# Optimization experiments

Measured on AMD Instinct MI355X. Metric: run time of the kernel, lower is better.

Reference implementation:

```python
import jax, jax.numpy as jnp
import numpy as np

GC_ALPHA = 3.0  # saturation factor in MTGNN-style graph constructor
TOP_K = 5       # ctor arg: GraphConstructor(n_classes, 5, dim)
EPS_NORM = 1e-12


def setup_inputs() -> dict:
    key = jax.random.key(0)
    k1, k2, k3, k4, k5 = jax.random.split(key, 5)
    B, C, H, W = 32, 384, 80, 80
    N = 27
    return {
        "x": jax.random.normal(k1, (B, C, H, W), dtype=jnp.float32),
        "alpha": jnp.ones((), dtype=jnp.float32),
        "clusters": jax.random.normal(k2, (N, C), dtype=jnp.float32),
        "gc_w1": jax.random.normal(k3, (C, C), dtype=jnp.float32) / np.sqrt(C),
        "gc_w2": jax.random.normal(k4, (C, C), dtype=jnp.float32) / np.sqrt(C),
        "gcn_w": jax.random.normal(k5, (C, C), dtype=jnp.float32) / np.sqrt(C),
    }


def _refine_clusters(clusters, gc_w1, gc_w2, gcn_w):
    # GraphConstructor: learned asymmetric adjacency over n_classes nodes, top-k sparsified
    n = clusters.shape[0]
    a = jnp.tanh(GC_ALPHA * (clusters @ gc_w1))          # [n, d]
    b = jnp.tanh(GC_ALPHA * (clusters @ gc_w2))          # [n, d]
    adj = jax.nn.relu(jnp.tanh(GC_ALPHA * (a @ b.T - b @ a.T)))  # [n, n]
    topv, _ = jax.lax.top_k(adj, TOP_K)
    A = jnp.where(adj >= topv[:, -1:], adj, 0.0)         # keep top-k per row
    # GCNConv (no bias): add self-loops, symmetric normalization
    A_hat = A + jnp.eye(n, dtype=A.dtype)
    dinv = 1.0 / jnp.sqrt(A_hat.sum(axis=1))
    A_norm = dinv[:, None] * A_hat * dinv[None, :]
    return A_norm @ (clusters @ gcn_w)                   # [n, d]


def reference(x, alpha, clusters, gc_w1, gc_w2, gcn_w):
    # mp=True path: refine codebook with tiny GCN over learned graph
    cl = _refine_clusters(clusters, gc_w1, gc_w2, gcn_w)
    # cosine similarity of per-pixel features against codebook
    nc = cl / jnp.maximum(jnp.linalg.norm(cl, axis=1, keepdims=True), EPS_NORM)
    nf = x / jnp.maximum(jnp.linalg.norm(x, axis=1, keepdims=True), EPS_NORM)
    inner_products = jnp.einsum('bchw,nc->bnhw', nf, nc)          # [B, n, H, W]
    cluster_probs = jax.nn.softmax(inner_products * alpha, axis=1)
    cluster_loss = -(cluster_probs * inner_products).sum(axis=1).mean()
    # entropy over unnormalized similarities (computed in original forward)
    p = jax.nn.softmax(jnp.einsum('bchw,nc->bnhw', x, clusters), axis=1)
    entropy = (-(p * jnp.log(p + 1e-10)).sum(axis=1)).mean()
    return cluster_loss, inner_products, cl, entropy
```

## Files before the change

kernel.cpp:

```cpp
#include <hip/hip_runtime.h>
#include <math.h>

#define N_CL   27
#define C_DIM  384
#define HW_SZ  6400
#define B_SZ   32
#define NPIX   (B_SZ*HW_SZ)
#define NTILE  3200
#define NCHUNK 12
#define WSF_PARTS 24576
#define WSF_ADJ   40000
#define ENT_OFF (1 + (size_t)NPIX*N_CL + (size_t)N_CL*C_DIM)

typedef unsigned short ushort_t;
using bf16x8 = __attribute__((ext_vector_type(8))) short;
using f32x4  = __attribute__((ext_vector_type(4))) float;

__device__ __forceinline__ float xla_tanh_f32(float x) {
    const float c = 7.99881172180175781f;
    if (fabsf(x) < 0.0004f) return x;
    const float xc = fminf(fmaxf(x, -c), c);
    const float x2 = xc*xc;
    float p = fmaf(x2, -2.76076847742355e-16f, 2.00018790482477e-13f);
    p = fmaf(x2, p, -8.60467152213735e-11f);
    p = fmaf(x2, p,  5.12229709037114e-08f);
    p = fmaf(x2, p,  1.48572235717979e-05f);
    p = fmaf(x2, p,  6.37261928875436e-04f);
    p = fmaf(x2, p,  4.89352455891786e-03f);
    p = xc*p;
    float q = fmaf(x2, 1.19825839466702e-06f, 1.18534705686654e-04f);
    q = fmaf(x2, q, 2.26843463243900e-03f);
    q = fmaf(x2, q, 4.89352518554385e-03f);
    return p/q;
}

__global__ __launch_bounds__(384) void cl_refine_mm(const float* __restrict__ clusters,
                                                    const float* __restrict__ w1,
                                                    const float* __restrict__ w2,
                                                    const float* __restrict__ w3,
                                                    float* __restrict__ ws) {
    const int i = blockIdx.x;
    const int m = blockIdx.y;
    const int j = threadIdx.x;
    __shared__ float crow[C_DIM];
    crow[j] = clusters[i*C_DIM + j];
    __syncthreads();
    const float* __restrict__ W = (m==0) ? w1 : (m==1) ? w2 : w3;
    float s0=0.f,s1=0.f,s2=0.f,s3=0.f;
    #pragma unroll 4
    for (int k=0;k<C_DIM;k+=4){
        s0 = fmaf(crow[k+0], W[(size_t)(k+0)*C_DIM + j], s0);
        s1 = fmaf(crow[k+1], W[(size_t)(k+1)*C_DIM + j], s1);
        s2 = fmaf(crow[k+2], W[(size_t)(k+2)*C_DIM + j], s2);
        s3 = fmaf(crow[k+3], W[(size_t)(k+3)*C_DIM + j], s3);
    }
    const float acc = (s0+s1)+(s2+s3);
    ws[(size_t)m*N_CL*C_DIM + i*C_DIM + j] = (m<2) ? xla_tanh_f32(3.0f*acc) : acc;
}

__global__ __launch_bounds__(64) void cl_adj(const float* __restrict__ ws,
                                             float* __restrict__ adj_out) {
    const float* __restrict__ Am = ws;
    const float* __restrict__ Bm = ws + N_CL*C_DIM;
    const int i = blockIdx.x / N_CL, j = blockIdx.x - (blockIdx.x / N_CL)*N_CL;
    const int lane = threadIdx.x;
    float p=0.f, q=0.f;
    #pragma unroll
    for (int e=0;e<6;e++){
        const int k = e*64 + lane;
        p = fmaf(Am[i*C_DIM+k], Bm[j*C_DIM+k], p);
        q = fmaf(Bm[i*C_DIM+k], Am[j*C_DIM+k], q);
    }
    float d = p - q;
    #pragma unroll
    for (int m=1;m<64;m<<=1) d += __shfl_xor(d, m);
    if (lane==0) adj_out[blockIdx.x] = fmaxf(xla_tanh_f32(3.0f*d), 0.f);
}

__global__ __launch_bounds__(1024) void cl_graph2(float* ws,
                                                  const float* __restrict__ clusters_g,
                                                  float* __restrict__ out) {
    const float* cg = ws + 2*N_CL*C_DIM;
    float* cl_out = out + 1 + (size_t)NPIX*N_CL;
    const int t = threadIdx.x;

    __shared__ float anorm[N_CL][N_CL+1];
    __shared__ float dinv[N_CL];
    __shared__ float rinv[N_CL];
    __shared__ float cls[N_CL][C_DIM];

    if (t < N_CL*N_CL) {
        const int i = t / N_CL, j = t - (t / N_CL)*N_CL;
        anorm[i][j] = ws[WSF_ADJ + t];
    }
    __syncthreads();
    if (t < N_CL) {
        unsigned mask=0; float thr=0.f;
        for (int s=0;s<5;s++){
            float bv=-1.f; int bi2=0;
            for (int j=0;j<N_CL;j++){
                if (mask & (1u<<j)) continue;
                const float v = anorm[t][j];
                if (v > bv){ bv=v; bi2=j; }
            }
            mask |= 1u<<bi2; thr = bv;
        }
        float rs=0.f;
        for (int j=0;j<N_CL;j++){
            float v = anorm[t][j];
            v = (v >= thr) ? v : 0.f;
            if (j==t) v += 1.f;
            anorm[t][j] = v;
            rs += v;
        }
        dinv[t] = 1.0f / sqrtf(rs);
    }
    __syncthreads();
    if (t < N_CL*N_CL) {
        const int i = t / N_CL, j = t - (t / N_CL)*N_CL;
        anorm[i][j] = dinv[i]*anorm[i][j]*dinv[j];
    }
    __syncthreads();
    for (int idx=t; idx<N_CL*C_DIM; idx+=1024){
        const int i = idx / C_DIM, d = idx - i*C_DIM;
        float s=0.f;
        #pragma unroll
        for (int j=0;j<N_CL;j++) s = fmaf(anorm[i][j], cg[(size_t)j*C_DIM + d], s);
        cls[i][d] = s;
        cl_out[idx] = s;
    }
    __syncthreads();
    if (t < N_CL) {
        float ssq=0.f;
        for (int d=0; d<C_DIM; d++){ const float v=cls[t][d]; ssq=fmaf(v,v,ssq); }
        rinv[t] = 1.0f / fmaxf(sqrtf(ssq), 1e-12f);
    }
    __syncthreads();
    ushort_t* wpk = (ushort_t*)ws;
    for (int idx=t; idx<64*C_DIM; idx+=1024){
        const int n = idx / C_DIM, k = idx - n*C_DIM;
        float v = 0.f;
        if (n < N_CL) v = cls[n][k] * rinv[n];
        else if (n >= 32 && n < 32+N_CL) v = clusters_g[(size_t)(n-32)*C_DIM + k];
        const unsigned bits = __float_as_uint(v);
        const ushort_t hi = (ushort_t)(bits >> 16);
        const float lof = v - __uint_as_float(bits & 0xFFFF0000u);
        const ushort_t lo = (ushort_t)(__float_as_uint(lof) >> 16);
        wpk[idx] = hi;
        wpk[64*C_DIM + idx] = lo;
    }
}

__global__ __launch_bounds__(256, 4) void cl_mfma(const float* __restrict__ x,
                                                  const float* __restrict__ alpha_p,
                                                  const ushort_t* __restrict__ wpk,
                                                  float* __restrict__ ws,
                                                  float* __restrict__ out) {
    __shared__ float    lA[2][64][33];
    __shared__ __align__(16) ushort_t lB[2][2][64][40];
    __shared__ float redL[4], redE[4];

    const int tid = threadIdx.x;
    const int blk = blockIdx.x;
    const int b   = blk / 100;
    const int hw0 = (blk - b*100) * 64;
    const float* __restrict__ xb = x + (size_t)b*C_DIM*HW_SZ + hw0;

    const int lane = tid & 63;
    const int w    = tid >> 6;
    const int l15  = lane & 15;
    const int g    = lane >> 4;
    const int k0   = g*8;
    const int apx  = w*16 + l15;

    const int a_kk = tid >> 4;
    const int a_px = (tid & 15) * 4;
    const int b_n  = tid >> 2;
    const int b_kb = (tid & 3) * 8;

    float4 ra0, ra1; uint4 rb0, rb1;
    #define LOADR(c) {                                                            \
        const int ch = (c)*32;                                                    \
        ra0 = *(const float4*)(xb + (size_t)(ch      + a_kk)*HW_SZ + a_px);       \
        ra1 = *(const float4*)(xb + (size_t)(ch + 16 + a_kk)*HW_SZ + a_px);       \
        rb0 = *(const uint4*)(wpk + (size_t)(     b_n)*C_DIM + ch + b_kb);        \
        rb1 = *(const uint4*)(wpk + (size_t)(64 + b_n)*C_DIM + ch + b_kb); }
    #define WRITE(bf) {                                                           \
        lA[bf][a_px+0][a_kk]    = ra0.x; lA[bf][a_px+1][a_kk]    = ra0.y;         \
        lA[bf][a_px+2][a_kk]    = ra0.z; lA[bf][a_px+3][a_kk]    = ra0.w;         \
        lA[bf][a_px+0][a_kk+16] = ra1.x; lA[bf][a_px+1][a_kk+16] = ra1.y;         \
        lA[bf][a_px+2][a_kk+16] = ra1.z; lA[bf][a_px+3][a_kk+16] = ra1.w;         \
        *(uint4*)(&lB[bf][0][b_n][b_kb]) = rb0;                                   \
        *(uint4*)(&lB[bf][1][b_n][b_kb]) = rb1; }

    f32x4 acc0={0,0,0,0}, acc1={0,0,0,0}, acc2={0,0,0,0}, acc3={0,0,0,0};
    float ss = 0.f;

    LOADR(0);
    WRITE(0);
    LOADR(1);
    __syncthreads();

    for (int c = 0; c < NCHUNK; c++) {
        const int cur = c & 1;
        union { ushort_t u[8]; bf16x8 v; } Ah, Al;
        #pragma unroll
        for (int e = 0; e < 8; e++) {
            const float xv = lA[cur][apx][k0 + e];
            const unsigned bits = __float_as_uint(xv);
            Ah.u[e] = (ushort_t)(bits >> 16);
            const float lof = xv - __uint_as_float(bits & 0xFFFF0000u);
            Al.u[e] = (ushort_t)(__float_as_uint(lof) >> 16);
            ss = fmaf(xv, xv, ss);
        }
        #pragma unroll
        for (int t = 0; t < 4; t++) {
            union { uint4 q; bf16x8 v; } Bh, Bl;
            Bh.q = *(const uint4*)(&lB[cur][0][t*16 + l15][k0]);
            Bl.q = *(const uint4*)(&lB[cur][1][t*16 + l15][k0]);
            f32x4 a;
            a = (t==0)?acc0:(t==1)?acc1:(t==2)?acc2:acc3;
            a = __builtin_amdgcn_mfma_f32_16x16x32_bf16(Ah.v, Bh.v, a, 0,0,0);
            a = __builtin_amdgcn_mfma_f32_16x16x32_bf16(Ah.v, Bl.v, a, 0,0,0);
            a = __builtin_amdgcn_mfma_f32_16x16x32_bf16(Al.v, Bh.v, a, 0,0,0);
            if (t==0) acc0=a; else if (t==1) acc1=a; else if (t==2) acc2=a; else acc3=a;
        }
        __syncthreads();
        if (c + 1 < NCHUNK) {
            WRITE(cur ^ 1);
            if (c + 2 < NCHUNK) LOADR(c+2);
            __syncthreads();
        }
    }

    ss += __shfl_xor(ss, 16);
    ss += __shfl_xor(ss, 32);
    f32x4 invv;
    #pragma unroll
    for (int r = 0; r < 4; r++) {
        const float s2 = __shfl(ss, g*4 + r);
        invv[r] = 1.0f / fmaxf(sqrtf(s2), 1e-12f);
    }

    const float alpha = alpha_p[0];
    float* __restrict__ out1 = out + 1;
    const int pxb = hw0 + w*16 + g*4;

    f32x4 st0, st1;
    #pragma unroll
    for (int r=0;r<4;r++){ st0[r] = acc0[r]*invv[r]; st1[r] = acc1[r]*invv[r]; }
    *(f32x4*)(out1 + (size_t)b*N_CL*HW_SZ + (size_t)l15*HW_SZ + pxb) = st0;
    if (l15 <= 10)
        *(f32x4*)(out1 + (size_t)b*N_CL*HW_SZ + (size_t)(16+l15)*HW_SZ + pxb) = st1;

    float wloss = 0.f, went = 0.f;
    #pragma unroll
    for (int r=0;r<4;r++){
        const float ip0 = st0[r], ip1 = st1[r];
        const float v0 = alpha*ip0;
        const float v1 = (l15<=10) ? alpha*ip1 : -INFINITY;
        float mx = fmaxf(v0, v1);
        #pragma unroll
        for (int m=1;m<16;m<<=1) mx = fmaxf(mx, __shfl_xor(mx, m));
        const float e0 = expf(v0 - mx);
        const float e1 = (l15<=10) ? expf(v1 - mx) : 0.f;
        float z = e0 + e1;
        float tt = fmaf(e0, ip0, (l15<=10) ? e1*ip1 : 0.f);
        #pragma unroll
        for (int m=1;m<16;m<<=1){ z += __shfl_xor(z,m); tt += __shfl_xor(tt,m); }
        wloss += tt/z;
        const float c0 = acc2[r];
        const float c1 = (l15<=10) ? acc3[r] : -INFINITY;
        float emx = fmaxf(c0, c1);
        #pragma unroll
        for (int m=1;m<16;m<<=1) emx = fmaxf(emx, __shfl_xor(emx, m));
        const float f0 = expf(c0 - emx);
        const float f1 = (l15<=10) ? expf(c1 - emx) : 0.f;
        float ez = f0 + f1;
        #pragma unroll
        for (int m=1;m<16;m<<=1) ez += __shfl_xor(ez,m);
        const float iz = 1.0f/ez;
        const float p0 = f0*iz, p1 = f1*iz;
        float te = -p0*logf(p0+1e-10f) - p1*logf(p1+1e-10f);
        #pragma unroll
        for (int m=1;m<16;m<<=1) te += __shfl_xor(te,m);
        went += te;
    }
    wloss += __shfl_xor(wloss,16); wloss += __shfl_xor(wloss,32);
    went  += __shfl_xor(went ,16); went  += __shfl_xor(went ,32);
    if (lane == 0) { redL[w] = wloss; redE[w] = went; }
    __syncthreads();
    if (tid == 0) {
        float* parts = ws + WSF_PARTS;
        parts[blk]         = redL[0]+redL[1]+redL[2]+redL[3];
        parts[NTILE + blk] = redE[0]+redE[1]+redE[2]+redE[3];
    }
}

__global__ __launch_bounds__(1024) void cl_final_reduce(const float* __restrict__ ws,
                                                        float* __restrict__ out) {
    __shared__ float r[1024];
    const int t = threadIdx.x;
    const float* parts = ws + WSF_PARTS;
    float s = 0.f;
    for (int j=t; j<NTILE; j+=1024) s += parts[j];
    r[t] = s; __syncthreads();
    for (int sft=512;sft>0;sft>>=1){ if (t<sft) r[t]+=r[t+sft]; __syncthreads(); }
    if (t==0) out[0] = -r[0]*(1.0f/NPIX);
    __syncthreads();
    s = 0.f;
    for (int j=t; j<NTILE; j+=1024) s += parts[NTILE + j];
    r[t] = s; __syncthreads();
    for (int sft=512;sft>0;sft>>=1){ if (t<sft) r[t]+=r[t+sft]; __syncthreads(); }
    if (t==0) out[ENT_OFF] = r[0]*(1.0f/NPIX);
}

extern "C" void kernel_launch(void* const* d_in, const int* in_sizes, int n_in,
                              void* d_out, int out_size, void* d_ws, size_t ws_size,
                              hipStream_t stream) {
    const float* x        = (const float*)d_in[0];
    const float* alpha    = (const float*)d_in[1];
    const float* clusters = (const float*)d_in[2];
    const float* w1       = (const float*)d_in[3];
    const float* w2       = (const float*)d_in[4];
    const float* w3       = (const float*)d_in[5];
    float* out = (float*)d_out;
    float* ws  = (float*)d_ws;

    cl_refine_mm<<<dim3(27,3), dim3(384), 0, stream>>>(clusters, w1, w2, w3, ws);
    cl_adj<<<dim3(N_CL*N_CL), dim3(64), 0, stream>>>(ws, ws + WSF_ADJ);
    cl_graph2<<<dim3(1), dim3(1024), 0, stream>>>(ws, clusters, out);
    cl_mfma<<<dim3(NTILE), dim3(256), 0, stream>>>(x, alpha, (const ushort_t*)ws, ws, out);
    cl_final_reduce<<<dim3(1), dim3(1024), 0, stream>>>(ws, out);
}
```

Before: 136.9 us.

## Load x activations directly into registers, bypassing LDS transpose staging

The x tile is no longer staged through a shared-memory transpose buffer. Each lane now loads its own 8 channel values per chunk straight from global memory into registers, using scalar strided loads that are coalesced across pixels. Only the weight tile is still staged in LDS, and the loop is unrolled by two with ping-pong register sets. This removes the LDS writes and reads for A and some bank conflicts, at the cost of more global load instructions (scalar instead of float4) and higher register pressure.

```diff
diff --git a/kernel.cpp b/kernel.cpp
--- a/kernel.cpp
+++ b/kernel.cpp
@@ -156,7 +156,6 @@
                                                   const ushort_t* __restrict__ wpk,
                                                   float* __restrict__ ws,
                                                   float* __restrict__ out) {
-    __shared__ float    lA[2][64][33];
     __shared__ __align__(16) ushort_t lB[2][2][64][40];
     __shared__ float redL[4], redE[4];
 
@@ -172,63 +171,75 @@
     const int g    = lane >> 4;
     const int k0   = g*8;
     const int apx  = w*16 + l15;
-
-    const int a_kk = tid >> 4;
-    const int a_px = (tid & 15) * 4;
+    const float* __restrict__ xl = xb + apx;
+
     const int b_n  = tid >> 2;
     const int b_kb = (tid & 3) * 8;
 
-    float4 ra0, ra1; uint4 rb0, rb1;
-    #define LOADR(c) {                                                            \
-        const int ch = (c)*32;                                                    \
-        ra0 = *(const float4*)(xb + (size_t)(ch      + a_kk)*HW_SZ + a_px);       \
-        ra1 = *(const float4*)(xb + (size_t)(ch + 16 + a_kk)*HW_SZ + a_px);       \
-        rb0 = *(const uint4*)(wpk + (size_t)(     b_n)*C_DIM + ch + b_kb);        \
-        rb1 = *(const uint4*)(wpk + (size_t)(64 + b_n)*C_DIM + ch + b_kb); }
-    #define WRITE(bf) {                                                           \
-        lA[bf][a_px+0][a_kk]    = ra0.x; lA[bf][a_px+1][a_kk]    = ra0.y;         \
-        lA[bf][a_px+2][a_kk]    = ra0.z; lA[bf][a_px+3][a_kk]    = ra0.w;         \
-        lA[bf][a_px+0][a_kk+16] = ra1.x; lA[bf][a_px+1][a_kk+16] = ra1.y;         \
-        lA[bf][a_px+2][a_kk+16] = ra1.z; lA[bf][a_px+3][a_kk+16] = ra1.w;         \
+    uint4 rb0, rb1;
+    #define LOADB(c) {                                                            \
+        rb0 = *(const uint4*)(wpk + (size_t)(     b_n)*C_DIM + (c)*32 + b_kb);    \
+        rb1 = *(const uint4*)(wpk + (size_t)(64 + b_n)*C_DIM + (c)*32 + b_kb); }
+    #define WRITEB(bf) {                                                          \
         *(uint4*)(&lB[bf][0][b_n][b_kb]) = rb0;                                   \
         *(uint4*)(&lB[bf][1][b_n][b_kb]) = rb1; }
 
+    #define LOADA(c, R0,R1,R2,R3,R4,R5,R6,R7) {                                   \
+        const float* pA = xl + (size_t)((c)*32 + k0)*HW_SZ;                       \
+        R0 = pA[0*HW_SZ]; R1 = pA[1*HW_SZ]; R2 = pA[2*HW_SZ]; R3 = pA[3*HW_SZ];  \
+        R4 = pA[4*HW_SZ]; R5 = pA[5*HW_SZ]; R6 = pA[6*HW_SZ]; R7 = pA[7*HW_SZ]; }
+
+    union { ushort_t u[8]; bf16x8 v; } Ah, Al;
+    float ss = 0.f;
+    #define CVT1(e, R) {                                                          \
+        const unsigned bits = __float_as_uint(R);                                 \
+        Ah.u[e] = (ushort_t)(bits >> 16);                                         \
+        const float lof = R - __uint_as_float(bits & 0xFFFF0000u);                \
+        Al.u[e] = (ushort_t)(__float_as_uint(lof) >> 16);                         \
+        ss = fmaf(R, R, ss); }
+    #define CONVERT(R0,R1,R2,R3,R4,R5,R6,R7) {                                    \
+        CVT1(0,R0) CVT1(1,R1) CVT1(2,R2) CVT1(3,R3)                               \
+        CVT1(4,R4) CVT1(5,R5) CVT1(6,R6) CVT1(7,R7) }
+
     f32x4 acc0={0,0,0,0}, acc1={0,0,0,0}, acc2={0,0,0,0}, acc3={0,0,0,0};
-    float ss = 0.f;
-
-    LOADR(0);
-    WRITE(0);
-    LOADR(1);
-    __syncthreads();
-
-    for (int c = 0; c < NCHUNK; c++) {
-        const int cur = c & 1;
-        union { ushort_t u[8]; bf16x8 v; } Ah, Al;
-        #pragma unroll
-        for (int e = 0; e < 8; e++) {
-            const float xv = lA[cur][apx][k0 + e];
-            const unsigned bits = __float_as_uint(xv);
-            Ah.u[e] = (ushort_t)(bits >> 16);
-            const float lof = xv - __uint_as_float(bits & 0xFFFF0000u);
-            Al.u[e] = (ushort_t)(__float_as_uint(lof) >> 16);
-            ss = fmaf(xv, xv, ss);
-        }
-        #pragma unroll
-        for (int t = 0; t < 4; t++) {
-            union { uint4 q; bf16x8 v; } Bh, Bl;
-            Bh.q = *(const uint4*)(&lB[cur][0][t*16 + l15][k0]);
-            Bl.q = *(const uint4*)(&lB[cur][1][t*16 + l15][k0]);
-            f32x4 a;
-            a = (t==0)?acc0:(t==1)?acc1:(t==2)?acc2:acc3;
-            a = __builtin_amdgcn_mfma_f32_16x16x32_bf16(Ah.v, Bh.v, a, 0,0,0);
-            a = __builtin_amdgcn_mfma_f32_16x16x32_bf16(Ah.v, Bl.v, a, 0,0,0);
-            a = __builtin_amdgcn_mfma_f32_16x16x32_bf16(Al.v, Bh.v, a, 0,0,0);
-            if (t==0) acc0=a; else if (t==1) acc1=a; else if (t==2) acc2=a; else acc3=a;
-        }
+    #define DOMFMA(cur) {                                                         \
+        _Pragma("unroll")                                                         \
+        for (int t = 0; t < 4; t++) {                                             \
+            union { uint4 q; bf16x8 v; } Bh, Bl;                                  \
+            Bh.q = *(const uint4*)(&lB[cur][0][t*16 + l15][k0]);                  \
+            Bl.q = *(const uint4*)(&lB[cur][1][t*16 + l15][k0]);                  \
+            f32x4 a = (t==0)?acc0:(t==1)?acc1:(t==2)?acc2:acc3;                   \
+            a = __builtin_amdgcn_mfma_f32_16x16x32_bf16(Ah.v, Bh.v, a, 0,0,0);    \
+            a = __builtin_amdgcn_mfma_f32_16x16x32_bf16(Ah.v, Bl.v, a, 0,0,0);    \
+            a = __builtin_amdgcn_mfma_f32_16x16x32_bf16(Al.v, Bh.v, a, 0,0,0);    \
+            if (t==0) acc0=a; else if (t==1) acc1=a; else if (t==2) acc2=a;       \
+            else acc3=a;                                                          \
+        } }
+
+    float Ra0,Ra1,Ra2,Ra3,Ra4,Ra5,Ra6,Ra7;
+    float Rb0,Rb1,Rb2,Rb3,Rb4,Rb5,Rb6,Rb7;
+
+    LOADA(0, Ra0,Ra1,Ra2,Ra3,Ra4,Ra5,Ra6,Ra7);
+    LOADB(0); WRITEB(0);
+    LOADA(1, Rb0,Rb1,Rb2,Rb3,Rb4,Rb5,Rb6,Rb7);
+    LOADB(1);
+    __syncthreads();
+
+    for (int cc = 0; cc < NCHUNK; cc += 2) {
+        CONVERT(Ra0,Ra1,Ra2,Ra3,Ra4,Ra5,Ra6,Ra7);
+        if (cc + 2 < NCHUNK) LOADA(cc+2, Ra0,Ra1,Ra2,Ra3,Ra4,Ra5,Ra6,Ra7);
+        DOMFMA(0);
         __syncthreads();
-        if (c + 1 < NCHUNK) {
-            WRITE(cur ^ 1);
-            if (c + 2 < NCHUNK) LOADR(c+2);
+        WRITEB(1);
+        if (cc + 2 < NCHUNK) LOADB(cc+2);
+        __syncthreads();
+        CONVERT(Rb0,Rb1,Rb2,Rb3,Rb4,Rb5,Rb6,Rb7);
+        if (cc + 3 < NCHUNK) LOADA(cc+3, Rb0,Rb1,Rb2,Rb3,Rb4,Rb5,Rb6,Rb7);
+        DOMFMA(1);
+        if (cc + 2 < NCHUNK) {
+            __syncthreads();
+            WRITEB(0);
+            if (cc + 3 < NCHUNK) LOADB(cc+3);
             __syncthreads();
         }
     }
```

Measured after the change: 136.6 us. About the same (-0.2%).
